# Performance work log

Hardware: AMD Instinct MI355X
Metric: run time of the kernel (lower is better)

## Reference

```python
import jax, jax.numpy as jnp
import numpy as np

N_NODES = 200000   # graph size
D = 128            # input feature dim
B = 1024           # seed batch
MAX_DEG = 128      # padded adjacency width
HID = 128          # aggregator output_dim (concat -> 2*HID)
N_CLASSES = 64
N_SAMPLES = (25, 10)  # fanout per hop (layer_specs n_train_samples)


def setup_inputs() -> dict:
    key = jax.random.key(0)
    ks = jax.random.split(key, 9)
    ids = jax.random.randint(ks[0], (B,), 0, N_NODES)
    feats = jax.random.normal(ks[1], (N_NODES, D), jnp.float32)
    adj = jax.random.randint(ks[2], (N_NODES, MAX_DEG), 0, N_NODES)
    init = lambda k, shp, fan: jax.random.normal(k, shp, jnp.float32) / np.float32(np.sqrt(fan))
    W_x1 = init(ks[3], (D, HID), D)
    W_n1 = init(ks[4], (D, HID), D)
    W_x2 = init(ks[5], (2 * HID, HID), 2 * HID)
    W_n2 = init(ks[6], (2 * HID, HID), 2 * HID)
    fc_w = init(ks[7], (2 * HID, N_CLASSES), 2 * HID)
    fc_b = jnp.zeros((N_CLASSES,), jnp.float32)
    return dict(ids=ids, feats=feats, adj=adj, W_x1=W_x1, W_n1=W_n1,
                W_x2=W_x2, W_n2=W_n2, fc_w=fc_w, fc_b=fc_b)


def _sample_ids(ids, adj):
    """Multi-hop uniform neighbor sampling (UniformNeighborSampler)."""
    key = jax.random.key(42)
    all_ids = [ids]
    cur = ids
    for i, n in enumerate(N_SAMPLES):
        k = jax.random.fold_in(key, i)
        cols = jax.random.randint(k, (cur.shape[0], n), 0, adj.shape[1])
        cur = adj[cur[:, None], cols].reshape(-1)  # [len(cur)*n]
        all_ids.append(cur)
    return all_ids


def _mean_agg(x, neibs, Wx, Wn, act):
    # neibs: [x.shape[0]*n_samples, d] -> mean over sampled neighbors
    agg = neibs.reshape(x.shape[0], -1, neibs.shape[1]).mean(axis=1)
    out = jnp.concatenate([x @ Wx, agg @ Wn], axis=1)  # bias-free Linears
    return jax.nn.relu(out) if act else out


def reference(ids, feats, adj, W_x1, W_n1, W_x2, W_n2, fc_w, fc_b):
    all_ids = _sample_ids(ids, adj)
    hs = [feats[i] for i in all_ids]  # gather: [B,d], [B*25,d], [B*250,d]
    hs = [_mean_agg(hs[k], hs[k + 1], W_x1, W_n1, True) for k in range(len(hs) - 1)]
    hs = [_mean_agg(hs[k], hs[k + 1], W_x2, W_n2, False) for k in range(len(hs) - 1)]
    out = hs[0]
    # F.normalize(out, dim=1) with eps=1e-12
    out = out / jnp.clip(jnp.linalg.norm(out, axis=1, keepdims=True), 1e-12)
    return out @ fc_w + fc_b
```

## Files before the change

### kernel.cpp

```cpp
#include <hip/hip_runtime.h>
#include <stdint.h>
#include <stddef.h>


typedef short bf16x8v __attribute__((ext_vector_type(8)));
typedef float f32x4v __attribute__((ext_vector_type(4)));

__host__ __device__ inline void tf2x32(uint32_t k0, uint32_t k1,
                                       uint32_t x0, uint32_t x1,
                                       uint32_t &o0, uint32_t &o1)
{
    uint32_t ks2 = k0 ^ k1 ^ 0x1BD11BDAu;
    uint32_t v0 = x0 + k0, v1 = x1 + k1;
#define TFR(d) { v0 += v1; v1 = (v1 << (d)) | (v1 >> (32 - (d))); v1 ^= v0; }
    TFR(13) TFR(15) TFR(26) TFR(6)   v0 += k1;  v1 += ks2 + 1u;
    TFR(17) TFR(29) TFR(16) TFR(24)  v0 += ks2; v1 += k0 + 2u;
    TFR(13) TFR(15) TFR(26) TFR(6)   v0 += k0;  v1 += k1 + 3u;
    TFR(17) TFR(29) TFR(16) TFR(24)  v0 += k1;  v1 += ks2 + 4u;
    TFR(13) TFR(15) TFR(26) TFR(6)   v0 += ks2; v1 += k0 + 5u;
#undef TFR
    o0 = v0; o1 = v1;
}

__device__ inline uint16_t f32_to_bf16_rne(float f)
{
    uint32_t u = __float_as_uint(f);
    u += 0x7FFFu + ((u >> 16) & 1u);
    return (uint16_t)(u >> 16);
}
__device__ inline float bf16_to_f32(uint16_t h)
{
    return __uint_as_float(((uint32_t)h) << 16);
}

__global__ void means_prep_kernel(const int* __restrict__ ids, const int* __restrict__ adj,
                                  const float* __restrict__ feats,
                                  const float* __restrict__ Wx1, const float* __restrict__ Wn1,
                                  uint16_t* __restrict__ xh, uint16_t* __restrict__ xl,
                                  uint16_t* __restrict__ nh, uint16_t* __restrict__ nl,
                                  uint32_t s0a, uint32_t s0b, uint32_t s1a, uint32_t s1b,
                                  int* __restrict__ ids1, float* __restrict__ m1,
                                  float* __restrict__ m0, float4* __restrict__ m2z)
{
    const int tid = threadIdx.x;
    const int bid = blockIdx.x;

    if (bid < 384) {
        int t = bid * 256 + tid;
        if (t < 32768) {
            int k = (t & 16383) >> 7, n = t & 127;
            const float* W = (t < 16384) ? Wx1 : Wn1;
            uint16_t* H = (t < 16384) ? xh : nh;
            uint16_t* L = (t < 16384) ? xl : nl;
            float v = W[k * 128 + n];
            uint16_t h = f32_to_bf16_rne(v);
            uint16_t l = f32_to_bf16_rne(v - bf16_to_f32(h));
            H[n * 128 + k] = h;
            L[n * 128 + k] = l;
        } else {
            m2z[t - 32768] = make_float4(0.f, 0.f, 0.f, 0.f);
        }
    }

    const int w = (bid * 256 + tid) >> 6;
    const int lane = tid & 63;
    if (w < 25600) {
        uint32_t h0, l0;
        tf2x32(s0a, s0b, 0u, (uint32_t)w, h0, l0);
        int s1idx = adj[(size_t)ids[w / 25] * 128u + ((h0 ^ l0) & 127u)];
        if (lane == 0) ids1[w] = s1idx;
        int idv = 0;
        if (lane < 10) {
            uint32_t h, l;
            tf2x32(s1a, s1b, 0u, (uint32_t)(w * 10 + lane), h, l);
            idv = adj[(size_t)s1idx * 128u + ((h ^ l) & 127u)];
        }
        float ax = 0.f, ay = 0.f;
#pragma unroll
        for (int t = 0; t < 10; ++t) {
            int id = __shfl(idv, t, 64);
            float2 v = *((const float2*)(feats + (size_t)id * 128) + lane);
            ax += v.x; ay += v.y;
        }
        *((float2*)(m1 + (size_t)w * 128) + lane) = make_float2(ax * 0.1f, ay * 0.1f);
    } else if (w < 26624) {
        int row = w - 25600;
        int s = ids[row];
        int idv = 0;
        if (lane < 25) {
            uint32_t h, l;
            tf2x32(s0a, s0b, 0u, (uint32_t)(row * 25 + lane), h, l);
            idv = adj[(size_t)s * 128u + ((h ^ l) & 127u)];
        }
        float ax = 0.f, ay = 0.f;
#pragma unroll
        for (int t = 0; t < 25; ++t) {
            int id = __shfl(idv, t, 64);
            float2 v = *((const float2*)(feats + (size_t)id * 128) + lane);
            ax += v.x; ay += v.y;
        }
        const float sc = 1.0f / 25.0f;
        *((float2*)(m0 + (size_t)row * 128) + lane) = make_float2(ax * sc, ay * sc);
    }
}

__launch_bounds__(256)
__global__ void gemm_l1_mfma(const float* __restrict__ feats,
                             const int* __restrict__ ids0, const int* __restrict__ ids1,
                             const float* __restrict__ m1, const float* __restrict__ m0,
                             const uint16_t* __restrict__ xh, const uint16_t* __restrict__ xl,
                             const uint16_t* __restrict__ nh, const uint16_t* __restrict__ nl,
                             float* __restrict__ m2, float* __restrict__ h10)
{
    const float* A; const int* g; const uint16_t* WH; const uint16_t* WL;
    int rows, ccol0;
    switch (blockIdx.z) {
    case 0:  A = feats; g = ids1;    WH = xh; WL = xl; rows = 25600; ccol0 = 0;   break;
    case 1:  A = m1;    g = nullptr; WH = nh; WL = nl; rows = 25600; ccol0 = 128; break;
    case 2:  A = feats; g = ids0;    WH = xh; WL = xl; rows = 1024;  ccol0 = 0;   break;
    default: A = m0;    g = nullptr; WH = nh; WL = nl; rows = 1024;  ccol0 = 128; break;
    }
    const int rb = blockIdx.x * 64;
    if (rb >= rows) return;
    const int nb0 = blockIdx.y * 64;

    __shared__ __align__(16) char smem[69632];
    uint16_t (*Ahi)[136] = reinterpret_cast<uint16_t(*)[136]>(smem);
    uint16_t (*Alo)[136] = reinterpret_cast<uint16_t(*)[136]>(smem + 17408);
    uint16_t (*Bhi)[136] = reinterpret_cast<uint16_t(*)[136]>(smem + 34816);
    uint16_t (*Blo)[136] = reinterpret_cast<uint16_t(*)[136]>(smem + 52224);

    const int tid = threadIdx.x;

#pragma unroll
    for (int i = 0; i < 8; ++i) {
        int s = tid + i * 256;
        int row = s >> 5, f4 = s & 31;
        int k0 = f4 * 4;
        size_t arow = g ? (size_t)g[rb + row] : (size_t)(rb + row);
        float4 v = *(const float4*)(A + arow * 128 + k0);
        uint16_t h0 = f32_to_bf16_rne(v.x), h1 = f32_to_bf16_rne(v.y);
        uint16_t h2 = f32_to_bf16_rne(v.z), h3 = f32_to_bf16_rne(v.w);
        *(ushort4*)&Ahi[row][k0] = make_ushort4(h0, h1, h2, h3);
        *(ushort4*)&Alo[row][k0] = make_ushort4(f32_to_bf16_rne(v.x - bf16_to_f32(h0)),
                                                f32_to_bf16_rne(v.y - bf16_to_f32(h1)),
                                                f32_to_bf16_rne(v.z - bf16_to_f32(h2)),
                                                f32_to_bf16_rne(v.w - bf16_to_f32(h3)));
    }
#pragma unroll
    for (int i = 0; i < 4; ++i) {
        int s = tid + i * 256;
        int n = s >> 4, ko = (s & 15) * 8;
        *(uint4*)&Bhi[n][ko] = *(const uint4*)(WH + (size_t)(nb0 + n) * 128 + ko);
        *(uint4*)&Blo[n][ko] = *(const uint4*)(WL + (size_t)(nb0 + n) * 128 + ko);
    }
    __syncthreads();

    const int lane = tid & 63;
    const int wv = tid >> 6;
    const int wm = (wv >> 1) * 32, wn = (wv & 1) * 32;
    const int fr = lane & 15;
    const int kb = lane >> 4;

    f32x4v acc[2][2] = {};
#pragma unroll
    for (int ks = 0; ks < 4; ++ks) {
        const int kk = ks * 32 + kb * 8;
        bf16x8v aH[2], aL[2], bH[2], bL[2];
#pragma unroll
        for (int mi = 0; mi < 2; ++mi) {
            aH[mi] = *(const bf16x8v*)&Ahi[wm + mi * 16 + fr][kk];
            aL[mi] = *(const bf16x8v*)&Alo[wm + mi * 16 + fr][kk];
        }
#pragma unroll
        for (int ni = 0; ni < 2; ++ni) {
            bH[ni] = *(const bf16x8v*)&Bhi[wn + ni * 16 + fr][kk];
            bL[ni] = *(const bf16x8v*)&Blo[wn + ni * 16 + fr][kk];
        }
#pragma unroll
        for (int mi = 0; mi < 2; ++mi)
#pragma unroll
            for (int ni = 0; ni < 2; ++ni) {
                acc[mi][ni] = __builtin_amdgcn_mfma_f32_16x16x32_bf16(aH[mi], bH[ni], acc[mi][ni], 0, 0, 0);
                acc[mi][ni] = __builtin_amdgcn_mfma_f32_16x16x32_bf16(aH[mi], bL[ni], acc[mi][ni], 0, 0, 0);
                acc[mi][ni] = __builtin_amdgcn_mfma_f32_16x16x32_bf16(aL[mi], bH[ni], acc[mi][ni], 0, 0, 0);
            }
    }

    if (blockIdx.z < 2) {
        __syncthreads();
        float (*Red)[68] = reinterpret_cast<float(*)[68]>(smem);
#pragma unroll
        for (int mi = 0; mi < 2; ++mi)
#pragma unroll
            for (int ni = 0; ni < 2; ++ni) {
                int rl = wm + mi * 16 + kb * 4;
                int cl = wn + ni * 16 + fr;
#pragma unroll
                for (int r = 0; r < 4; ++r)
                    Red[rl + r][cl] = fmaxf(acc[mi][ni][r], 0.0f);
            }
        __syncthreads();
        int col = tid & 63, gs = tid >> 6;
        int gg = rb / 25 + gs;
        int rs = max(gg * 25, rb), re = min(gg * 25 + 25, rb + 64);
        if (rs < re) {
            float s = 0.f;
            for (int r = rs; r < re; ++r) s += Red[r - rb][col];
            atomicAdd(&m2[(size_t)gg * 256 + ccol0 + nb0 + col], s * (1.0f / 25.0f));
        }
    } else {
#pragma unroll
        for (int mi = 0; mi < 2; ++mi)
#pragma unroll
            for (int ni = 0; ni < 2; ++ni) {
                int orow = rb + wm + mi * 16 + kb * 4;
                int ocol = ccol0 + nb0 + wn + ni * 16 + fr;
#pragma unroll
                for (int r = 0; r < 4; ++r)
                    h10[(size_t)(orow + r) * 256 + ocol] = fmaxf(acc[mi][ni][r], 0.0f);
            }
    }
}

__launch_bounds__(256)
__global__ void tail_kernel(const float* __restrict__ h10, const float* __restrict__ m2,
                            const float* __restrict__ Wx2, const float* __restrict__ Wn2,
                            const float* __restrict__ fcw, const float* __restrict__ fcb,
                            float* __restrict__ out)
{
    __shared__ float X[4][260];
    __shared__ float M[4][260];
    __shared__ float H[4][260];
    const int tid = threadIdx.x;
    const int r0 = blockIdx.x * 4;

    {
        int r = tid >> 6, q = tid & 63;
        *(float4*)&X[r][q * 4] = *((const float4*)(h10 + (size_t)(r0 + r) * 256) + q);
        *(float4*)&M[r][q * 4] = *((const float4*)(m2 + (size_t)(r0 + r) * 256) + q);
    }
    __syncthreads();

    {
        const float* W = (tid < 128) ? Wx2 : Wn2;
        const float (*S)[260] = (tid < 128) ? X : M;
        int c = tid & 127;
        float acc0 = 0.f, acc1 = 0.f, acc2 = 0.f, acc3 = 0.f;
        for (int k4 = 0; k4 < 256; k4 += 4) {
            float4 s0 = *(const float4*)&S[0][k4];
            float4 s1 = *(const float4*)&S[1][k4];
            float4 s2 = *(const float4*)&S[2][k4];
            float4 s3 = *(const float4*)&S[3][k4];
            float w0 = W[(size_t)(k4 + 0) * 128 + c];
            float w1 = W[(size_t)(k4 + 1) * 128 + c];
            float w2 = W[(size_t)(k4 + 2) * 128 + c];
            float w3 = W[(size_t)(k4 + 3) * 128 + c];
            acc0 = fmaf(s0.x, w0, fmaf(s0.y, w1, fmaf(s0.z, w2, fmaf(s0.w, w3, acc0))));
            acc1 = fmaf(s1.x, w0, fmaf(s1.y, w1, fmaf(s1.z, w2, fmaf(s1.w, w3, acc1))));
            acc2 = fmaf(s2.x, w0, fmaf(s2.y, w1, fmaf(s2.z, w2, fmaf(s2.w, w3, acc2))));
            acc3 = fmaf(s3.x, w0, fmaf(s3.y, w1, fmaf(s3.z, w2, fmaf(s3.w, w3, acc3))));
        }
        H[0][tid] = acc0; H[1][tid] = acc1; H[2][tid] = acc2; H[3][tid] = acc3;
    }
    __syncthreads();

    const int w = tid >> 6, lane = tid & 63;
    float4 hv = *((const float4*)&H[w][0] + lane);
    float ss = hv.x * hv.x + hv.y * hv.y + hv.z * hv.z + hv.w * hv.w;
#pragma unroll
    for (int o = 32; o > 0; o >>= 1) ss += __shfl_xor(ss, o, 64);
    float scale = 1.0f / fmaxf(sqrtf(ss), 1e-12f);

    float acc = 0.f;
    for (int k4 = 0; k4 < 256; k4 += 4) {
        float4 h4 = *(const float4*)&H[w][k4];
        acc = fmaf(h4.x, fcw[(size_t)(k4 + 0) * 64 + lane],
              fmaf(h4.y, fcw[(size_t)(k4 + 1) * 64 + lane],
              fmaf(h4.z, fcw[(size_t)(k4 + 2) * 64 + lane],
              fmaf(h4.w, fcw[(size_t)(k4 + 3) * 64 + lane], acc))));
    }
    out[(size_t)(r0 + w) * 64 + lane] = acc * scale + fcb[lane];
}

extern "C" void kernel_launch(void* const* d_in, const int* in_sizes, int n_in,
                              void* d_out, int out_size, void* d_ws, size_t ws_size,
                              hipStream_t stream)
{
    const int*   ids   = (const int*)d_in[0];
    const float* feats = (const float*)d_in[1];
    const int*   adj   = (const int*)d_in[2];
    const float* W_x1  = (const float*)d_in[3];
    const float* W_n1  = (const float*)d_in[4];
    const float* W_x2  = (const float*)d_in[5];
    const float* W_n2  = (const float*)d_in[6];
    const float* fc_w  = (const float*)d_in[7];
    const float* fc_b  = (const float*)d_in[8];
    float* out = (float*)d_out;

    char* ws = (char*)d_ws;
    int*      ids1 = (int*)(ws + 0);
    float*    m1   = (float*)(ws + 102400);
    float*    m0   = (float*)(ws + 13209600);
    float*    h10  = (float*)(ws + 39948288);
    float*    m2   = (float*)(ws + 40996864);
    uint16_t* xh   = (uint16_t*)(ws + 43094016);
    uint16_t* xl   = (uint16_t*)(ws + 43126784);
    uint16_t* nh   = (uint16_t*)(ws + 43159552);
    uint16_t* nl   = (uint16_t*)(ws + 43192320);

    uint32_t f0a, f0b, f1a, f1b, s0a, s0b, s1a, s1b;
    tf2x32(0u, 42u, 0u, 0u, f0a, f0b);
    tf2x32(0u, 42u, 0u, 1u, f1a, f1b);
    tf2x32(f0a, f0b, 0u, 1u, s0a, s0b);
    tf2x32(f1a, f1b, 0u, 1u, s1a, s1b);

    means_prep_kernel<<<6656, 256, 0, stream>>>(ids, adj, feats, W_x1, W_n1,
                                                xh, xl, nh, nl,
                                                s0a, s0b, s1a, s1b,
                                                ids1, m1, m0, (float4*)m2);
    gemm_l1_mfma<<<dim3(400, 2, 4), 256, 0, stream>>>(feats, ids, ids1, m1, m0,
                                                      xh, xl, nh, nl, m2, h10);
    tail_kernel<<<256, 256, 0, stream>>>(h10, m2, W_x2, W_n2, fc_w, fc_b, out);
}
```

Measured before the change: 70.29 us.

## Fuse neighbor mean aggregation into GEMM A-tile load, read weights from global

The prologue now only samples neighbor ids (ids1, ids2), splits the weights and zeroes m2. The feature gathers and neighbor means move into the GEMM kernel, which builds its bf16 hi/lo A tiles in shared memory. This removes the m1/m0 fp32 intermediates that were written to and read back from global memory. Each block now computes all 128 output columns instead of 64, so the gathered rows are used once rather than twice. B fragments are read straight from global/L2 instead of being staged in LDS, which halves shared memory but adds global-load latency inside the MFMA loop and puts serial gathers on the GEMM's critical path.

```diff
diff --git a/kernel.cpp b/kernel.cpp
--- a/kernel.cpp
+++ b/kernel.cpp
@@ -33,167 +33,160 @@
     return __uint_as_float(((uint32_t)h) << 16);
 }
 
-__global__ void means_prep_kernel(const int* __restrict__ ids, const int* __restrict__ adj,
-                                  const float* __restrict__ feats,
-                                  const float* __restrict__ Wx1, const float* __restrict__ Wn1,
-                                  uint16_t* __restrict__ xh, uint16_t* __restrict__ xl,
-                                  uint16_t* __restrict__ nh, uint16_t* __restrict__ nl,
-                                  uint32_t s0a, uint32_t s0b, uint32_t s1a, uint32_t s1b,
-                                  int* __restrict__ ids1, float* __restrict__ m1,
-                                  float* __restrict__ m0, float4* __restrict__ m2z)
-{
-    const int tid = threadIdx.x;
-    const int bid = blockIdx.x;
-
-    if (bid < 384) {
-        int t = bid * 256 + tid;
-        if (t < 32768) {
-            int k = (t & 16383) >> 7, n = t & 127;
-            const float* W = (t < 16384) ? Wx1 : Wn1;
-            uint16_t* H = (t < 16384) ? xh : nh;
-            uint16_t* L = (t < 16384) ? xl : nl;
-            float v = W[k * 128 + n];
-            uint16_t h = f32_to_bf16_rne(v);
-            uint16_t l = f32_to_bf16_rne(v - bf16_to_f32(h));
-            H[n * 128 + k] = h;
-            L[n * 128 + k] = l;
-        } else {
-            m2z[t - 32768] = make_float4(0.f, 0.f, 0.f, 0.f);
-        }
-    }
-
-    const int w = (bid * 256 + tid) >> 6;
-    const int lane = tid & 63;
-    if (w < 25600) {
+__global__ void prologue_kernel(const int* __restrict__ ids, const int* __restrict__ adj,
+                                const float* __restrict__ Wx1, const float* __restrict__ Wn1,
+                                uint16_t* __restrict__ xh, uint16_t* __restrict__ xl,
+                                uint16_t* __restrict__ nh, uint16_t* __restrict__ nl,
+                                uint32_t s0a, uint32_t s0b, uint32_t s1a, uint32_t s1b,
+                                int* __restrict__ ids1, int* __restrict__ ids2,
+                                float4* __restrict__ m2z)
+{
+    int t = blockIdx.x * 256 + threadIdx.x;
+    if (t < 32768) {
+        int k = (t & 16383) >> 7, n = t & 127;
+        const float* W = (t < 16384) ? Wx1 : Wn1;
+        uint16_t* H = (t < 16384) ? xh : nh;
+        uint16_t* L = (t < 16384) ? xl : nl;
+        float v = W[k * 128 + n];
+        uint16_t h = f32_to_bf16_rne(v);
+        uint16_t l = f32_to_bf16_rne(v - bf16_to_f32(h));
+        H[n * 128 + k] = h;
+        L[n * 128 + k] = l;
+    } else if (t < 98304) {
+        m2z[t - 32768] = make_float4(0.f, 0.f, 0.f, 0.f);
+    } else if (t < 123904) {
+        int j = t - 98304;
+        uint32_t h, l;
+        tf2x32(s0a, s0b, 0u, (uint32_t)j, h, l);
+        ids1[j] = adj[(size_t)ids[j / 25] * 128u + ((h ^ l) & 127u)];
+    } else if (t < 379904) {
+        int j = t - 123904;
         uint32_t h0, l0;
-        tf2x32(s0a, s0b, 0u, (uint32_t)w, h0, l0);
-        int s1idx = adj[(size_t)ids[w / 25] * 128u + ((h0 ^ l0) & 127u)];
-        if (lane == 0) ids1[w] = s1idx;
-        int idv = 0;
-        if (lane < 10) {
-            uint32_t h, l;
-            tf2x32(s1a, s1b, 0u, (uint32_t)(w * 10 + lane), h, l);
-            idv = adj[(size_t)s1idx * 128u + ((h ^ l) & 127u)];
-        }
-        float ax = 0.f, ay = 0.f;
-#pragma unroll
-        for (int t = 0; t < 10; ++t) {
-            int id = __shfl(idv, t, 64);
-            float2 v = *((const float2*)(feats + (size_t)id * 128) + lane);
-            ax += v.x; ay += v.y;
-        }
-        *((float2*)(m1 + (size_t)w * 128) + lane) = make_float2(ax * 0.1f, ay * 0.1f);
-    } else if (w < 26624) {
-        int row = w - 25600;
-        int s = ids[row];
-        int idv = 0;
-        if (lane < 25) {
-            uint32_t h, l;
-            tf2x32(s0a, s0b, 0u, (uint32_t)(row * 25 + lane), h, l);
-            idv = adj[(size_t)s * 128u + ((h ^ l) & 127u)];
-        }
-        float ax = 0.f, ay = 0.f;
-#pragma unroll
-        for (int t = 0; t < 25; ++t) {
-            int id = __shfl(idv, t, 64);
-            float2 v = *((const float2*)(feats + (size_t)id * 128) + lane);
-            ax += v.x; ay += v.y;
-        }
-        const float sc = 1.0f / 25.0f;
-        *((float2*)(m0 + (size_t)row * 128) + lane) = make_float2(ax * sc, ay * sc);
+        tf2x32(s0a, s0b, 0u, (uint32_t)(j / 10), h0, l0);
+        int a1 = adj[(size_t)ids[j / 250] * 128u + ((h0 ^ l0) & 127u)];
+        uint32_t h1, l1;
+        tf2x32(s1a, s1b, 0u, (uint32_t)j, h1, l1);
+        ids2[j] = adj[(size_t)a1 * 128u + ((h1 ^ l1) & 127u)];
     }
 }
 
 __launch_bounds__(256)
-__global__ void gemm_l1_mfma(const float* __restrict__ feats,
-                             const int* __restrict__ ids0, const int* __restrict__ ids1,
-                             const float* __restrict__ m1, const float* __restrict__ m0,
-                             const uint16_t* __restrict__ xh, const uint16_t* __restrict__ xl,
-                             const uint16_t* __restrict__ nh, const uint16_t* __restrict__ nl,
-                             float* __restrict__ m2, float* __restrict__ h10)
-{
-    const float* A; const int* g; const uint16_t* WH; const uint16_t* WL;
-    int rows, ccol0;
-    switch (blockIdx.z) {
-    case 0:  A = feats; g = ids1;    WH = xh; WL = xl; rows = 25600; ccol0 = 0;   break;
-    case 1:  A = m1;    g = nullptr; WH = nh; WL = nl; rows = 25600; ccol0 = 128; break;
-    case 2:  A = feats; g = ids0;    WH = xh; WL = xl; rows = 1024;  ccol0 = 0;   break;
-    default: A = m0;    g = nullptr; WH = nh; WL = nl; rows = 1024;  ccol0 = 128; break;
-    }
-    const int rb = blockIdx.x * 64;
-    if (rb >= rows) return;
-    const int nb0 = blockIdx.y * 64;
-
-    __shared__ __align__(16) char smem[69632];
+__global__ void gemm_mega(const float* __restrict__ feats, const int* __restrict__ ids,
+                          const int* __restrict__ ids1, const int* __restrict__ ids2,
+                          const uint16_t* __restrict__ xh, const uint16_t* __restrict__ xl,
+                          const uint16_t* __restrict__ nh, const uint16_t* __restrict__ nl,
+                          float* __restrict__ m2, float* __restrict__ h10)
+{
+    __shared__ __align__(16) char smem[34816];
     uint16_t (*Ahi)[136] = reinterpret_cast<uint16_t(*)[136]>(smem);
     uint16_t (*Alo)[136] = reinterpret_cast<uint16_t(*)[136]>(smem + 17408);
-    uint16_t (*Bhi)[136] = reinterpret_cast<uint16_t(*)[136]>(smem + 34816);
-    uint16_t (*Blo)[136] = reinterpret_cast<uint16_t(*)[136]>(smem + 52224);
 
     const int tid = threadIdx.x;
-
-#pragma unroll
-    for (int i = 0; i < 8; ++i) {
-        int s = tid + i * 256;
-        int row = s >> 5, f4 = s & 31;
-        int k0 = f4 * 4;
-        size_t arow = g ? (size_t)g[rb + row] : (size_t)(rb + row);
-        float4 v = *(const float4*)(A + arow * 128 + k0);
-        uint16_t h0 = f32_to_bf16_rne(v.x), h1 = f32_to_bf16_rne(v.y);
-        uint16_t h2 = f32_to_bf16_rne(v.z), h3 = f32_to_bf16_rne(v.w);
-        *(ushort4*)&Ahi[row][k0] = make_ushort4(h0, h1, h2, h3);
-        *(ushort4*)&Alo[row][k0] = make_ushort4(f32_to_bf16_rne(v.x - bf16_to_f32(h0)),
-                                                f32_to_bf16_rne(v.y - bf16_to_f32(h1)),
-                                                f32_to_bf16_rne(v.z - bf16_to_f32(h2)),
-                                                f32_to_bf16_rne(v.w - bf16_to_f32(h3)));
-    }
-#pragma unroll
-    for (int i = 0; i < 4; ++i) {
-        int s = tid + i * 256;
-        int n = s >> 4, ko = (s & 15) * 8;
-        *(uint4*)&Bhi[n][ko] = *(const uint4*)(WH + (size_t)(nb0 + n) * 128 + ko);
-        *(uint4*)&Blo[n][ko] = *(const uint4*)(WL + (size_t)(nb0 + n) * 128 + ko);
-    }
-    __syncthreads();
+    const int vb = blockIdx.x;
+    int z, bx;
+    if (vb < 16)      { z = 3; bx = vb; }
+    else if (vb < 32) { z = 2; bx = vb - 16; }
+    else              { int q = vb - 32; z = q & 1; bx = q >> 1; }
+    const int rb = bx * 64;
+    const bool isX = (z == 0) || (z == 2);
+    const uint16_t* WH = isX ? xh : nh;
+    const uint16_t* WL = isX ? xl : nl;
+    const int ccol0 = isX ? 0 : 128;
 
     const int lane = tid & 63;
     const int wv = tid >> 6;
-    const int wm = (wv >> 1) * 32, wn = (wv & 1) * 32;
+
+    if (z == 0 || z == 2) {
+        const int* g = (z == 0) ? ids1 : ids;
+#pragma unroll
+        for (int i = 0; i < 8; ++i) {
+            int s = tid + i * 256;
+            int row = s >> 5, f4 = s & 31, k0 = f4 * 4;
+            size_t arow = (size_t)g[rb + row];
+            float4 v = *(const float4*)(feats + arow * 128 + k0);
+            uint16_t h0 = f32_to_bf16_rne(v.x), h1 = f32_to_bf16_rne(v.y);
+            uint16_t h2 = f32_to_bf16_rne(v.z), h3 = f32_to_bf16_rne(v.w);
+            *(ushort4*)&Ahi[row][k0] = make_ushort4(h0, h1, h2, h3);
+            *(ushort4*)&Alo[row][k0] = make_ushort4(f32_to_bf16_rne(v.x - bf16_to_f32(h0)),
+                                                    f32_to_bf16_rne(v.y - bf16_to_f32(h1)),
+                                                    f32_to_bf16_rne(v.z - bf16_to_f32(h2)),
+                                                    f32_to_bf16_rne(v.w - bf16_to_f32(h3)));
+        }
+    } else if (z == 1) {
+        for (int i = 0; i < 16; ++i) {
+            int r = wv * 16 + i;
+            int w = rb + r;
+            int idv = (lane < 10) ? ids2[w * 10 + lane] : 0;
+            float ax = 0.f, ay = 0.f;
+#pragma unroll
+            for (int t = 0; t < 10; ++t) {
+                int id = __shfl(idv, t, 64);
+                float2 v = *((const float2*)(feats + (size_t)id * 128) + lane);
+                ax += v.x; ay += v.y;
+            }
+            ax *= 0.1f; ay *= 0.1f;
+            uint16_t hx = f32_to_bf16_rne(ax), hy = f32_to_bf16_rne(ay);
+            *(ushort2*)&Ahi[r][lane * 2] = make_ushort2(hx, hy);
+            *(ushort2*)&Alo[r][lane * 2] = make_ushort2(f32_to_bf16_rne(ax - bf16_to_f32(hx)),
+                                                        f32_to_bf16_rne(ay - bf16_to_f32(hy)));
+        }
+    } else {
+        for (int i = 0; i < 16; ++i) {
+            int r = wv * 16 + i;
+            int row = rb + r;
+            int idv = (lane < 25) ? ids1[row * 25 + lane] : 0;
+            float ax = 0.f, ay = 0.f;
+#pragma unroll
+            for (int t = 0; t < 25; ++t) {
+                int id = __shfl(idv, t, 64);
+                float2 v = *((const float2*)(feats + (size_t)id * 128) + lane);
+                ax += v.x; ay += v.y;
+            }
+            ax *= (1.0f / 25.0f); ay *= (1.0f / 25.0f);
+            uint16_t hx = f32_to_bf16_rne(ax), hy = f32_to_bf16_rne(ay);
+            *(ushort2*)&Ahi[r][lane * 2] = make_ushort2(hx, hy);
+            *(ushort2*)&Alo[r][lane * 2] = make_ushort2(f32_to_bf16_rne(ax - bf16_to_f32(hx)),
+                                                        f32_to_bf16_rne(ay - bf16_to_f32(hy)));
+        }
+    }
+    __syncthreads();
+
+    const int wm = (wv >> 1) * 32;
+    const int wn = (wv & 1) * 64;
     const int fr = lane & 15;
     const int kb = lane >> 4;
 
-    f32x4v acc[2][2] = {};
+    f32x4v acc[2][4] = {};
 #pragma unroll
     for (int ks = 0; ks < 4; ++ks) {
         const int kk = ks * 32 + kb * 8;
-        bf16x8v aH[2], aL[2], bH[2], bL[2];
+        bf16x8v aH[2], aL[2];
 #pragma unroll
         for (int mi = 0; mi < 2; ++mi) {
             aH[mi] = *(const bf16x8v*)&Ahi[wm + mi * 16 + fr][kk];
             aL[mi] = *(const bf16x8v*)&Alo[wm + mi * 16 + fr][kk];
         }
 #pragma unroll
-        for (int ni = 0; ni < 2; ++ni) {
-            bH[ni] = *(const bf16x8v*)&Bhi[wn + ni * 16 + fr][kk];
-            bL[ni] = *(const bf16x8v*)&Blo[wn + ni * 16 + fr][kk];
-        }
+        for (int ni = 0; ni < 4; ++ni) {
+            size_t wrow = (size_t)(wn + ni * 16 + fr) * 128 + kk;
+            bf16x8v bH = *(const bf16x8v*)(WH + wrow);
+            bf16x8v bL = *(const bf16x8v*)(WL + wrow);
+#pragma unroll
+            for (int mi = 0; mi < 2; ++mi) {
+                acc[mi][ni] = __builtin_amdgcn_mfma_f32_16x16x32_bf16(aH[mi], bH, acc[mi][ni], 0, 0, 0);
+                acc[mi][ni] = __builtin_amdgcn_mfma_f32_16x16x32_bf16(aH[mi], bL, acc[mi][ni], 0, 0, 0);
+                acc[mi][ni] = __builtin_amdgcn_mfma_f32_16x16x32_bf16(aL[mi], bH, acc[mi][ni], 0, 0, 0);
+            }
+        }
+    }
+
+    if (z < 2) {
+        __syncthreads();
+        float (*Red)[132] = reinterpret_cast<float(*)[132]>(smem);
 #pragma unroll
         for (int mi = 0; mi < 2; ++mi)
 #pragma unroll
-            for (int ni = 0; ni < 2; ++ni) {
-                acc[mi][ni] = __builtin_amdgcn_mfma_f32_16x16x32_bf16(aH[mi], bH[ni], acc[mi][ni], 0, 0, 0);
-                acc[mi][ni] = __builtin_amdgcn_mfma_f32_16x16x32_bf16(aH[mi], bL[ni], acc[mi][ni], 0, 0, 0);
-                acc[mi][ni] = __builtin_amdgcn_mfma_f32_16x16x32_bf16(aL[mi], bH[ni], acc[mi][ni], 0, 0, 0);
-            }
-    }
-
-    if (blockIdx.z < 2) {
-        __syncthreads();
-        float (*Red)[68] = reinterpret_cast<float(*)[68]>(smem);
-#pragma unroll
-        for (int mi = 0; mi < 2; ++mi)
-#pragma unroll
-            for (int ni = 0; ni < 2; ++ni) {
+            for (int ni = 0; ni < 4; ++ni) {
                 int rl = wm + mi * 16 + kb * 4;
                 int cl = wn + ni * 16 + fr;
 #pragma unroll
@@ -201,21 +194,20 @@
                     Red[rl + r][cl] = fmaxf(acc[mi][ni][r], 0.0f);
             }
         __syncthreads();
-        int col = tid & 63, gs = tid >> 6;
-        int gg = rb / 25 + gs;
-        int rs = max(gg * 25, rb), re = min(gg * 25 + 25, rb + 64);
-        if (rs < re) {
+        int col = tid & 127;
+        for (int gg = rb / 25 + (tid >> 7); gg * 25 < rb + 64; gg += 2) {
+            int rs = max(gg * 25, rb), re = min(gg * 25 + 25, rb + 64);
             float s = 0.f;
             for (int r = rs; r < re; ++r) s += Red[r - rb][col];
-            atomicAdd(&m2[(size_t)gg * 256 + ccol0 + nb0 + col], s * (1.0f / 25.0f));
+            atomicAdd(&m2[(size_t)gg * 256 + ccol0 + col], s * (1.0f / 25.0f));
         }
     } else {
 #pragma unroll
         for (int mi = 0; mi < 2; ++mi)
 #pragma unroll
-            for (int ni = 0; ni < 2; ++ni) {
+            for (int ni = 0; ni < 4; ++ni) {
                 int orow = rb + wm + mi * 16 + kb * 4;
-                int ocol = ccol0 + nb0 + wn + ni * 16 + fr;
+                int ocol = ccol0 + wn + ni * 16 + fr;
 #pragma unroll
                 for (int r = 0; r < 4; ++r)
                     h10[(size_t)(orow + r) * 256 + ocol] = fmaxf(acc[mi][ni][r], 0.0f);
@@ -300,14 +292,13 @@
 
     char* ws = (char*)d_ws;
     int*      ids1 = (int*)(ws + 0);
-    float*    m1   = (float*)(ws + 102400);
-    float*    m0   = (float*)(ws + 13209600);
-    float*    h10  = (float*)(ws + 39948288);
-    float*    m2   = (float*)(ws + 40996864);
-    uint16_t* xh   = (uint16_t*)(ws + 43094016);
-    uint16_t* xl   = (uint16_t*)(ws + 43126784);
-    uint16_t* nh   = (uint16_t*)(ws + 43159552);
-    uint16_t* nl   = (uint16_t*)(ws + 43192320);
+    int*      ids2 = (int*)(ws + 102400);
+    float*    h10  = (float*)(ws + 1126400);
+    float*    m2   = (float*)(ws + 2174976);
+    uint16_t* xh   = (uint16_t*)(ws + 3223552);
+    uint16_t* xl   = (uint16_t*)(ws + 3256320);
+    uint16_t* nh   = (uint16_t*)(ws + 3289088);
+    uint16_t* nl   = (uint16_t*)(ws + 3321856);
 
     uint32_t f0a, f0b, f1a, f1b, s0a, s0b, s1a, s1b;
     tf2x32(0u, 42u, 0u, 0u, f0a, f0b);
@@ -315,11 +306,11 @@
     tf2x32(f0a, f0b, 0u, 1u, s0a, s0b);
     tf2x32(f1a, f1b, 0u, 1u, s1a, s1b);
 
-    means_prep_kernel<<<6656, 256, 0, stream>>>(ids, adj, feats, W_x1, W_n1,
-                                                xh, xl, nh, nl,
-                                                s0a, s0b, s1a, s1b,
-                                                ids1, m1, m0, (float4*)m2);
-    gemm_l1_mfma<<<dim3(400, 2, 4), 256, 0, stream>>>(feats, ids, ids1, m1, m0,
-                                                      xh, xl, nh, nl, m2, h10);
+    prologue_kernel<<<1484, 256, 0, stream>>>(ids, adj, W_x1, W_n1,
+                                              xh, xl, nh, nl,
+                                              s0a, s0b, s1a, s1b,
+                                              ids1, ids2, (float4*)m2);
+    gemm_mega<<<832, 256, 0, stream>>>(feats, ids, ids1, ids2,
+                                       xh, xl, nh, nl, m2, h10);
     tail_kernel<<<256, 256, 0, stream>>>(h10, m2, W_x2, W_n2, fc_w, fc_b, out);
 }
```

Measured after the change: 80.21 us. 14.1% more time.
